# Optimization experiments

Measured on AMD Instinct MI355X. Metric: run time of the kernel, lower is better.

## Reference

```python
import jax, jax.numpy as jnp
import numpy as np

N = 131072
DIM = 16      # irrep dim of Rs_in == Rs_out (mul 4 of l=0,1)
YDIM = 9      # sum(2l+1) for l_filters {0,1,2}
NPATH = 96    # mul_dim of Rs_f (radial channels)
NPATH0 = 32   # linear (l=0) paths
HID = 64      # radial MLP hidden width


def _sh(u):
    """Real spherical harmonics for l=0,1,2 on unit vectors u[N,3] -> Y[9, N]."""
    x, y, z = u[:, 0], u[:, 1], u[:, 2]
    c0 = 0.28209479177387814
    c1 = 0.4886025119029199
    c2 = 1.0925484305920792
    return jnp.stack([
        jnp.full_like(x, c0),
        c1 * y, c1 * z, c1 * x,
        c2 * x * y,
        c2 * y * z,
        0.31539156525252005 * (3.0 * z * z - 1.0),
        c2 * x * z,
        0.5462742152960396 * (x * x - y * y),
    ])  # [YDIM, N]


def setup_inputs() -> dict:
    key = jax.random.key(0)
    ks = jax.random.split(key, 8)
    return {
        "r": jax.random.normal(ks[0], (N, 3), jnp.float32),
        "mixing_matrix1": jax.random.normal(ks[1], (DIM, DIM, YDIM, NPATH), jnp.float32) * 0.1,
        "mixing_matrix2": jax.random.normal(ks[2], (DIM, DIM, NPATH0), jnp.float32) * 0.1,
        "weight": jax.random.normal(ks[3], (NPATH0,), jnp.float32),
        "W1": jax.random.normal(ks[4], (1, HID), jnp.float32),
        "b1": jnp.zeros((HID,), jnp.float32),
        "W2": jax.random.normal(ks[5], (HID, NPATH), jnp.float32) / 8.0,
        "b2": jnp.zeros((NPATH,), jnp.float32),
    }


def reference(r, mixing_matrix1, mixing_matrix2, weight, W1, b1, W2, b2):
    r_eps = 0.0
    radii = jnp.linalg.norm(r, axis=1)                 # [N]
    mask = radii > r_eps                               # [N]
    u = r / jnp.maximum(radii, 1e-12)[:, None]         # unit vectors
    Y = _sh(u)                                         # [YDIM, N]
    # radial MLP: R -> R^NPATH
    h = jax.nn.relu(radii[:, None] @ W1 + b1)          # [N, HID]
    R = h @ W2 + b2                                    # [N, NPATH]
    # kernel1 = einsum('ijyw,yz,zw->zij'): outer(Y,R) per point, then one GEMM
    F = jnp.einsum('yz,zw->zyw', Y, R).reshape(-1, YDIM * NPATH)   # [N, y*w]
    k1 = (F @ mixing_matrix1.reshape(DIM * DIM, YDIM * NPATH).T).reshape(-1, DIM, DIM)
    # kernel2 = einsum('ijk,k->ij')
    k2 = jnp.einsum('ijk,k->ij', mixing_matrix2, weight)           # [DIM, DIM]
    # scatter: radii>eps gets kernel1, radii<=eps gets kernel2 (jit-safe select)
    return jnp.where(mask[:, None, None], k1, k2[None, :, :])      # [N, DIM, DIM]
```

## Files before the change

kernel.cpp:

```cpp
#include <hip/hip_runtime.h>
#include <math.h>

#define NPTS   131072
#define DIMC   256
#define YD     9
#define NPATHS 96
#define NPATH0 32
#define HID    64
#define NREG   65
#define QSTR   18

typedef float f32x4 __attribute__((ext_vector_type(4)));


__global__ __launch_bounds__(256) void precompute_kernel(
    const float* __restrict__ W1, const float* __restrict__ b1,
    const float* __restrict__ W2, const float* __restrict__ b2,
    const float* __restrict__ M1, const float* __restrict__ M2,
    const float* __restrict__ wgt,
    float* __restrict__ Q, float* __restrict__ xout, float* __restrict__ k2out)
{
    const int j   = blockIdx.x / 3;
    const int ys  = blockIdx.x % 3;
    const int tid = threadIdx.x;
    __shared__ __align__(16) float sx[HID];
    __shared__ __align__(16) float sa[HID], sb[HID];
    __shared__ __align__(16) float ssa[HID], ssb[HID];
    __shared__ __align__(16) float sv[NPATHS], sc[NPATHS];

    if (tid < HID) {
        float a = W1[tid], b = b1[tid];
        sa[tid] = a; sb[tid] = b;
        bool flips = (a > 0.f && b < 0.f) || (a < 0.f && b > 0.f);
        sx[tid] = flips ? (-b / a) : __builtin_inff();
    }
    __syncthreads();
    if (tid < HID) {
        float a = sa[tid], b = sb[tid], xh = sx[tid];
        int rank = 0;
        for (int k = 0; k < HID; ++k) {
            float xk = sx[k];
            rank += (xk < xh || (xk == xh && k < tid)) ? 1 : 0;
        }
        bool base = (b > 0.f) || (b == 0.f && a > 0.f);
        bool sig  = base ^ (rank < j);
        ssa[tid] = sig ? a : 0.f;
        ssb[tid] = sig ? b : 0.f;
    }
    __syncthreads();
    if (tid < NPATHS) {
        float vv = 0.f, cc = 0.f;
        for (int h = 0; h < HID; ++h) {
            float w2 = W2[h * NPATHS + tid];
            vv += ssa[h] * w2;
            cc += ssb[h] * w2;
        }
        sv[tid] = vv;
        sc[tid] = cc + b2[tid];
    }
    __syncthreads();
    {
        const int c  = tid;
        const int y0 = ys * 3;
        float accP[3] = {0.f, 0.f, 0.f};
        float accD[3] = {0.f, 0.f, 0.f};
        for (int w4 = 0; w4 < NPATHS / 4; ++w4) {
            float4 v4 = ((const float4*)sv)[w4];
            float4 c4 = ((const float4*)sc)[w4];
            #pragma unroll
            for (int e = 0; e < 3; ++e) {
                const float4 m4 = *(const float4*)(M1 + (size_t)(c * YD + y0 + e) * NPATHS + w4 * 4);
                accP[e] += m4.x * v4.x + m4.y * v4.y + m4.z * v4.z + m4.w * v4.w;
                accD[e] += m4.x * c4.x + m4.y * c4.y + m4.z * c4.z + m4.w * c4.w;
            }
        }
        float* qrow = Q + ((size_t)j * DIMC + c) * QSTR;
        #pragma unroll
        for (int e = 0; e < 3; ++e) {
            qrow[y0 + e]     = accP[e];
            qrow[9 + y0 + e] = accD[e];
        }
    }
    if (j == 0 && ys == 0) {
        if (tid < HID) xout[tid] = sx[tid];
        float s = 0.f;
        #pragma unroll
        for (int k = 0; k < NPATH0; ++k) s += M2[tid * NPATH0 + k] * wgt[k];
        k2out[tid] = s;
    }
}

__global__ __launch_bounds__(256, 2) void main_kernel(
    const float* __restrict__ r, const float* __restrict__ Q,
    const float* __restrict__ xflip, const float* __restrict__ k2,
    float* __restrict__ out)
{
    __shared__ __align__(16) float qArr[64 * 20];
    __shared__ int sUni, sJJ0;
    const int tid = threadIdx.x;
    const int n0  = blockIdx.x * 64;

    if (tid < 64) {
        const int n = n0 + tid;
        float rx = r[(size_t)n * 3 + 0];
        float ry = r[(size_t)n * 3 + 1];
        float rz = r[(size_t)n * 3 + 2];
        float t  = sqrtf(rx * rx + ry * ry + rz * rz);
        float rcp = 1.f / fmaxf(t, 1e-12f);
        float ux = rx * rcp, uy = ry * rcp, uz = rz * rcp;
        const float c0 = 0.28209479177387814f;
        const float c1 = 0.4886025119029199f;
        const float c2 = 1.0925484305920792f;
        float Y[9];
        Y[0] = c0;
        Y[1] = c1 * uy;
        Y[2] = c1 * uz;
        Y[3] = c1 * ux;
        Y[4] = c2 * ux * uy;
        Y[5] = c2 * uy * uz;
        Y[6] = 0.31539156525252005f * (3.f * uz * uz - 1.f);
        Y[7] = c2 * ux * uz;
        Y[8] = 0.5462742152960396f * (ux * ux - uy * uy);
        int jj = 0;
        for (int h = 0; h < HID; ++h) jj += (xflip[h] < t) ? 1 : 0;
        float* q = qArr + tid * 20;
        #pragma unroll
        for (int y = 0; y < 9; ++y) { q[y] = t * Y[y]; q[9 + y] = Y[y]; }
        q[18] = (float)jj;
        q[19] = (t > 0.f) ? 1.f : 0.f;
        int jj0 = __shfl(jj, 0, 64);
        unsigned long long bal = __ballot(jj == jj0);
        if (tid == 0) { sUni = (bal == 0xFFFFFFFFFFFFFFFFULL) ? 1 : 0; sJJ0 = jj0; }
    }
    __syncthreads();

    const int cg  = tid & 63;
    const int pg  = tid >> 6;
    const int c0i = cg * 4;
    const float4 k2v = *(const float4*)(k2 + c0i);
    const int pbeg = pg * 16;

    if (sUni) {
        const float4* cb = (const float4*)(Q + ((size_t)sJJ0 * DIMC + c0i) * QSTR);
        float cfs[72];
        #pragma unroll
        for (int v = 0; v < 18; ++v) {
            float4 t4 = cb[v];
            cfs[v * 4 + 0] = t4.x; cfs[v * 4 + 1] = t4.y;
            cfs[v * 4 + 2] = t4.z; cfs[v * 4 + 3] = t4.w;
        }
        for (int p = pbeg; p < pbeg + 16; ++p) {
            const float4* qv = (const float4*)(qArr + p * 20);
            float4 a0 = qv[0], a1 = qv[1], a2 = qv[2], a3 = qv[3], a4 = qv[4];
            float acc0, acc1, acc2, acc3;
            acc0  = a0.x * cfs[ 0] + a0.y * cfs[ 1] + a0.z * cfs[ 2] + a0.w * cfs[ 3];
            acc0 += a1.x * cfs[ 4] + a1.y * cfs[ 5] + a1.z * cfs[ 6] + a1.w * cfs[ 7];
            acc0 += a2.x * cfs[ 8] + a2.y * cfs[ 9] + a2.z * cfs[10] + a2.w * cfs[11];
            acc0 += a3.x * cfs[12] + a3.y * cfs[13] + a3.z * cfs[14] + a3.w * cfs[15];
            acc0 += a4.x * cfs[16] + a4.y * cfs[17];
            acc1  = a0.x * cfs[18] + a0.y * cfs[19] + a0.z * cfs[20] + a0.w * cfs[21];
            acc1 += a1.x * cfs[22] + a1.y * cfs[23] + a1.z * cfs[24] + a1.w * cfs[25];
            acc1 += a2.x * cfs[26] + a2.y * cfs[27] + a2.z * cfs[28] + a2.w * cfs[29];
            acc1 += a3.x * cfs[30] + a3.y * cfs[31] + a3.z * cfs[32] + a3.w * cfs[33];
            acc1 += a4.x * cfs[34] + a4.y * cfs[35];
            acc2  = a0.x * cfs[36] + a0.y * cfs[37] + a0.z * cfs[38] + a0.w * cfs[39];
            acc2 += a1.x * cfs[40] + a1.y * cfs[41] + a1.z * cfs[42] + a1.w * cfs[43];
            acc2 += a2.x * cfs[44] + a2.y * cfs[45] + a2.z * cfs[46] + a2.w * cfs[47];
            acc2 += a3.x * cfs[48] + a3.y * cfs[49] + a3.z * cfs[50] + a3.w * cfs[51];
            acc2 += a4.x * cfs[52] + a4.y * cfs[53];
            acc3  = a0.x * cfs[54] + a0.y * cfs[55] + a0.z * cfs[56] + a0.w * cfs[57];
            acc3 += a1.x * cfs[58] + a1.y * cfs[59] + a1.z * cfs[60] + a1.w * cfs[61];
            acc3 += a2.x * cfs[62] + a2.y * cfs[63] + a2.z * cfs[64] + a2.w * cfs[65];
            acc3 += a3.x * cfs[66] + a3.y * cfs[67] + a3.z * cfs[68] + a3.w * cfs[69];
            acc3 += a4.x * cfs[70] + a4.y * cfs[71];
            const bool msk = (a4.w != 0.f);
            f32x4 o;
            o.x = msk ? acc0 : k2v.x;
            o.y = msk ? acc1 : k2v.y;
            o.z = msk ? acc2 : k2v.z;
            o.w = msk ? acc3 : k2v.w;
            __builtin_nontemporal_store(o, (f32x4*)(out + (size_t)(n0 + p) * DIMC + c0i));
        }
    } else {
        float cfs[72];
        int curj = -1;
        for (int p = pbeg; p < pbeg + 16; ++p) {
            const float4* qv = (const float4*)(qArr + p * 20);
            float4 a0 = qv[0], a1 = qv[1], a2 = qv[2], a3 = qv[3], a4 = qv[4];
            int jj = (int)a4.z;
            if (jj != curj) {
                curj = jj;
                const float4* cb = (const float4*)(Q + ((size_t)jj * DIMC + c0i) * QSTR);
                #pragma unroll
                for (int v = 0; v < 18; ++v) {
                    float4 t4 = cb[v];
                    cfs[v * 4 + 0] = t4.x; cfs[v * 4 + 1] = t4.y;
                    cfs[v * 4 + 2] = t4.z; cfs[v * 4 + 3] = t4.w;
                }
            }
            float qs[18] = { a0.x, a0.y, a0.z, a0.w,  a1.x, a1.y, a1.z, a1.w,
                             a2.x, a2.y, a2.z, a2.w,  a3.x, a3.y, a3.z, a3.w,
                             a4.x, a4.y };
            float acc0 = 0.f, acc1 = 0.f, acc2 = 0.f, acc3 = 0.f;
            #pragma unroll
            for (int i = 0; i < 18; ++i) {
                acc0 += qs[i] * cfs[0 * 18 + i];
                acc1 += qs[i] * cfs[1 * 18 + i];
                acc2 += qs[i] * cfs[2 * 18 + i];
                acc3 += qs[i] * cfs[3 * 18 + i];
            }
            const bool msk = (a4.w != 0.f);
            float4 o;
            o.x = msk ? acc0 : k2v.x;
            o.y = msk ? acc1 : k2v.y;
            o.z = msk ? acc2 : k2v.z;
            o.w = msk ? acc3 : k2v.w;
            *(float4*)(out + (size_t)(n0 + p) * DIMC + c0i) = o;
        }
    }
}

extern "C" void kernel_launch(void* const* d_in, const int* in_sizes, int n_in,
                              void* d_out, int out_size, void* d_ws, size_t ws_size,
                              hipStream_t stream)
{
    const float* r   = (const float*)d_in[0];
    const float* M1  = (const float*)d_in[1];
    const float* M2  = (const float*)d_in[2];
    const float* wgt = (const float*)d_in[3];
    const float* W1  = (const float*)d_in[4];
    const float* b1  = (const float*)d_in[5];
    const float* W2  = (const float*)d_in[6];
    const float* b2  = (const float*)d_in[7];
    float* out = (float*)d_out;

    float* ws = (float*)d_ws;
    float* Q  = ws;
    float* xf = ws + (size_t)NREG * DIMC * QSTR;
    float* k2 = xf + HID;

    precompute_kernel<<<NREG * 3, 256, 0, stream>>>(W1, b1, W2, b2, M1, M2, wgt, Q, xf, k2);
    main_kernel<<<NPTS / 64, 256, 0, stream>>>(r, Q, xf, k2, out);
}
```

Before: 186.7 us.

## Transpose Q layout, coalesce precompute with shuffle reductions, prefetch coefficients before barrier

Precompute now has 8 lanes cooperatively dot each M1 row with the slope and intercept vectors, reduce with xor shuffles, and write Q in a transposed [region][y][channel] layout. The main kernel reads coefficients as coalesced float4 strided loads, speculatively loads region-0 coefficients before the barrier to overlap with the per-point setup, and caches flip points in LDS. It also raises the occupancy hint to 3 blocks per SM and uses nontemporal stores on the non-uniform path. The risk is extra register pressure from the higher launch bound and a wasted load when region 0 is not the one used.

Result: no change. 188.6 us (+1.0%).

```diff
diff --git a/kernel.cpp b/kernel.cpp
--- a/kernel.cpp
+++ b/kernel.cpp
@@ -20,9 +20,9 @@
     const float* __restrict__ wgt,
     float* __restrict__ Q, float* __restrict__ xout, float* __restrict__ k2out)
 {
-    const int j   = blockIdx.x / 3;
-    const int ys  = blockIdx.x % 3;
-    const int tid = threadIdx.x;
+    const int j    = blockIdx.x >> 2;
+    const int rblk = blockIdx.x & 3;
+    const int tid  = threadIdx.x;
     __shared__ __align__(16) float sx[HID];
     __shared__ __align__(16) float sa[HID], sb[HID];
     __shared__ __align__(16) float ssa[HID], ssb[HID];
@@ -59,29 +59,44 @@
         sc[tid] = cc + b2[tid];
     }
     __syncthreads();
+
     {
-        const int c  = tid;
-        const int y0 = ys * 3;
-        float accP[3] = {0.f, 0.f, 0.f};
-        float accD[3] = {0.f, 0.f, 0.f};
-        for (int w4 = 0; w4 < NPATHS / 4; ++w4) {
-            float4 v4 = ((const float4*)sv)[w4];
-            float4 c4 = ((const float4*)sc)[w4];
-            #pragma unroll
-            for (int e = 0; e < 3; ++e) {
-                const float4 m4 = *(const float4*)(M1 + (size_t)(c * YD + y0 + e) * NPATHS + w4 * 4);
-                accP[e] += m4.x * v4.x + m4.y * v4.y + m4.z * v4.z + m4.w * v4.w;
-                accD[e] += m4.x * c4.x + m4.y * c4.y + m4.z * c4.z + m4.w * c4.w;
-            }
-        }
-        float* qrow = Q + ((size_t)j * DIMC + c) * QSTR;
-        #pragma unroll
-        for (int e = 0; e < 3; ++e) {
-            qrow[y0 + e]     = accP[e];
-            qrow[9 + y0 + e] = accD[e];
-        }
-    }
-    if (j == 0 && ys == 0) {
+        const int g    = tid >> 3;
+        const int lane = tid & 7;
+        const float4 v0 = *(const float4*)(sv + lane * 4);
+        const float4 v1 = *(const float4*)(sv + lane * 4 + 32);
+        const float4 v2 = *(const float4*)(sv + lane * 4 + 64);
+        const float4 d0 = *(const float4*)(sc + lane * 4);
+        const float4 d1 = *(const float4*)(sc + lane * 4 + 32);
+        const float4 d2 = *(const float4*)(sc + lane * 4 + 64);
+        const int row0 = rblk * (2304 / 4);
+        for (int it = 0; it < (2304 / 4) / 32; ++it) {
+            const int row = row0 + it * 32 + g;
+            const float* mrow = M1 + (size_t)row * NPATHS + lane * 4;
+            float4 m0 = *(const float4*)(mrow);
+            float4 m1 = *(const float4*)(mrow + 32);
+            float4 m2 = *(const float4*)(mrow + 64);
+            float p = m0.x*v0.x + m0.y*v0.y + m0.z*v0.z + m0.w*v0.w
+                    + m1.x*v1.x + m1.y*v1.y + m1.z*v1.z + m1.w*v1.w
+                    + m2.x*v2.x + m2.y*v2.y + m2.z*v2.z + m2.w*v2.w;
+            float d = m0.x*d0.x + m0.y*d0.y + m0.z*d0.z + m0.w*d0.w
+                    + m1.x*d1.x + m1.y*d1.y + m1.z*d1.z + m1.w*d1.w
+                    + m2.x*d2.x + m2.y*d2.y + m2.z*d2.z + m2.w*d2.w;
+            #pragma unroll
+            for (int off = 1; off < 8; off <<= 1) {
+                p += __shfl_xor(p, off, 64);
+                d += __shfl_xor(d, off, 64);
+            }
+            if (lane == 0) {
+                const int c = row / 9;
+                const int y = row - c * 9;
+                Q[((size_t)j * QSTR + y)     * DIMC + c] = p;
+                Q[((size_t)j * QSTR + 9 + y) * DIMC + c] = d;
+            }
+        }
+    }
+
+    if (blockIdx.x == 0) {
         if (tid < HID) xout[tid] = sx[tid];
         float s = 0.f;
         #pragma unroll
@@ -90,17 +105,22 @@
     }
 }
 
-__global__ __launch_bounds__(256, 2) void main_kernel(
+__global__ __launch_bounds__(256, 3) void main_kernel(
     const float* __restrict__ r, const float* __restrict__ Q,
     const float* __restrict__ xflip, const float* __restrict__ k2,
     float* __restrict__ out)
 {
     __shared__ __align__(16) float qArr[64 * 20];
+    __shared__ __align__(16) float sxf[64];
     __shared__ int sUni, sJJ0;
     const int tid = threadIdx.x;
     const int n0  = blockIdx.x * 64;
+    const int cg  = tid & 63;
+    const int pg  = tid >> 6;
+    const int c0i = cg * 4;
 
     if (tid < 64) {
+        sxf[tid] = xflip[tid];
         const int n = n0 + tid;
         float rx = r[(size_t)n * 3 + 0];
         float ry = r[(size_t)n * 3 + 1];
@@ -121,58 +141,62 @@
         Y[6] = 0.31539156525252005f * (3.f * uz * uz - 1.f);
         Y[7] = c2 * ux * uz;
         Y[8] = 0.5462742152960396f * (ux * ux - uy * uy);
+        float* q = qArr + tid * 20;
+        #pragma unroll
+        for (int y = 0; y < 9; ++y) { q[y] = t * Y[y]; q[9 + y] = Y[y]; }
+        q[19] = (t > 0.f) ? 1.f : 0.f;
         int jj = 0;
-        for (int h = 0; h < HID; ++h) jj += (xflip[h] < t) ? 1 : 0;
-        float* q = qArr + tid * 20;
-        #pragma unroll
-        for (int y = 0; y < 9; ++y) { q[y] = t * Y[y]; q[9 + y] = Y[y]; }
+        #pragma unroll
+        for (int h4 = 0; h4 < 16; ++h4) {
+            float4 x4 = ((const float4*)sxf)[h4];
+            jj += (x4.x < t ? 1 : 0) + (x4.y < t ? 1 : 0)
+                + (x4.z < t ? 1 : 0) + (x4.w < t ? 1 : 0);
+        }
         q[18] = (float)jj;
-        q[19] = (t > 0.f) ? 1.f : 0.f;
         int jj0 = __shfl(jj, 0, 64);
         unsigned long long bal = __ballot(jj == jj0);
         if (tid == 0) { sUni = (bal == 0xFFFFFFFFFFFFFFFFULL) ? 1 : 0; sJJ0 = jj0; }
     }
-    __syncthreads();
-
-    const int cg  = tid & 63;
-    const int pg  = tid >> 6;
-    const int c0i = cg * 4;
+
+    float cfs[72];
+    {
+        const float4* cb = (const float4*)Q + cg;
+        #pragma unroll
+        for (int v = 0; v < 18; ++v) {
+            float4 t4 = cb[v * 64];
+            cfs[v * 4 + 0] = t4.x; cfs[v * 4 + 1] = t4.y;
+            cfs[v * 4 + 2] = t4.z; cfs[v * 4 + 3] = t4.w;
+        }
+    }
+    __syncthreads();
+
     const float4 k2v = *(const float4*)(k2 + c0i);
     const int pbeg = pg * 16;
 
     if (sUni) {
-        const float4* cb = (const float4*)(Q + ((size_t)sJJ0 * DIMC + c0i) * QSTR);
-        float cfs[72];
-        #pragma unroll
-        for (int v = 0; v < 18; ++v) {
-            float4 t4 = cb[v];
-            cfs[v * 4 + 0] = t4.x; cfs[v * 4 + 1] = t4.y;
-            cfs[v * 4 + 2] = t4.z; cfs[v * 4 + 3] = t4.w;
+        if (sJJ0 != 0) {
+            const float4* cb = (const float4*)(Q + (size_t)sJJ0 * QSTR * DIMC) + cg;
+            #pragma unroll
+            for (int v = 0; v < 18; ++v) {
+                float4 t4 = cb[v * 64];
+                cfs[v * 4 + 0] = t4.x; cfs[v * 4 + 1] = t4.y;
+                cfs[v * 4 + 2] = t4.z; cfs[v * 4 + 3] = t4.w;
+            }
         }
         for (int p = pbeg; p < pbeg + 16; ++p) {
             const float4* qv = (const float4*)(qArr + p * 20);
             float4 a0 = qv[0], a1 = qv[1], a2 = qv[2], a3 = qv[3], a4 = qv[4];
-            float acc0, acc1, acc2, acc3;
-            acc0  = a0.x * cfs[ 0] + a0.y * cfs[ 1] + a0.z * cfs[ 2] + a0.w * cfs[ 3];
-            acc0 += a1.x * cfs[ 4] + a1.y * cfs[ 5] + a1.z * cfs[ 6] + a1.w * cfs[ 7];
-            acc0 += a2.x * cfs[ 8] + a2.y * cfs[ 9] + a2.z * cfs[10] + a2.w * cfs[11];
-            acc0 += a3.x * cfs[12] + a3.y * cfs[13] + a3.z * cfs[14] + a3.w * cfs[15];
-            acc0 += a4.x * cfs[16] + a4.y * cfs[17];
-            acc1  = a0.x * cfs[18] + a0.y * cfs[19] + a0.z * cfs[20] + a0.w * cfs[21];
-            acc1 += a1.x * cfs[22] + a1.y * cfs[23] + a1.z * cfs[24] + a1.w * cfs[25];
-            acc1 += a2.x * cfs[26] + a2.y * cfs[27] + a2.z * cfs[28] + a2.w * cfs[29];
-            acc1 += a3.x * cfs[30] + a3.y * cfs[31] + a3.z * cfs[32] + a3.w * cfs[33];
-            acc1 += a4.x * cfs[34] + a4.y * cfs[35];
-            acc2  = a0.x * cfs[36] + a0.y * cfs[37] + a0.z * cfs[38] + a0.w * cfs[39];
-            acc2 += a1.x * cfs[40] + a1.y * cfs[41] + a1.z * cfs[42] + a1.w * cfs[43];
-            acc2 += a2.x * cfs[44] + a2.y * cfs[45] + a2.z * cfs[46] + a2.w * cfs[47];
-            acc2 += a3.x * cfs[48] + a3.y * cfs[49] + a3.z * cfs[50] + a3.w * cfs[51];
-            acc2 += a4.x * cfs[52] + a4.y * cfs[53];
-            acc3  = a0.x * cfs[54] + a0.y * cfs[55] + a0.z * cfs[56] + a0.w * cfs[57];
-            acc3 += a1.x * cfs[58] + a1.y * cfs[59] + a1.z * cfs[60] + a1.w * cfs[61];
-            acc3 += a2.x * cfs[62] + a2.y * cfs[63] + a2.z * cfs[64] + a2.w * cfs[65];
-            acc3 += a3.x * cfs[66] + a3.y * cfs[67] + a3.z * cfs[68] + a3.w * cfs[69];
-            acc3 += a4.x * cfs[70] + a4.y * cfs[71];
+            const float qs[18] = { a0.x, a0.y, a0.z, a0.w,  a1.x, a1.y, a1.z, a1.w,
+                                   a2.x, a2.y, a2.z, a2.w,  a3.x, a3.y, a3.z, a3.w,
+                                   a4.x, a4.y };
+            float acc0 = 0.f, acc1 = 0.f, acc2 = 0.f, acc3 = 0.f;
+            #pragma unroll
+            for (int v = 0; v < 18; ++v) {
+                acc0 += qs[v] * cfs[v * 4 + 0];
+                acc1 += qs[v] * cfs[v * 4 + 1];
+                acc2 += qs[v] * cfs[v * 4 + 2];
+                acc3 += qs[v] * cfs[v * 4 + 3];
+            }
             const bool msk = (a4.w != 0.f);
             f32x4 o;
             o.x = msk ? acc0 : k2v.x;
@@ -182,40 +206,39 @@
             __builtin_nontemporal_store(o, (f32x4*)(out + (size_t)(n0 + p) * DIMC + c0i));
         }
     } else {
-        float cfs[72];
-        int curj = -1;
+        int curj = 0;
         for (int p = pbeg; p < pbeg + 16; ++p) {
             const float4* qv = (const float4*)(qArr + p * 20);
             float4 a0 = qv[0], a1 = qv[1], a2 = qv[2], a3 = qv[3], a4 = qv[4];
             int jj = (int)a4.z;
             if (jj != curj) {
                 curj = jj;
-                const float4* cb = (const float4*)(Q + ((size_t)jj * DIMC + c0i) * QSTR);
+                const float4* cb = (const float4*)(Q + (size_t)jj * QSTR * DIMC) + cg;
                 #pragma unroll
                 for (int v = 0; v < 18; ++v) {
-                    float4 t4 = cb[v];
+                    float4 t4 = cb[v * 64];
                     cfs[v * 4 + 0] = t4.x; cfs[v * 4 + 1] = t4.y;
                     cfs[v * 4 + 2] = t4.z; cfs[v * 4 + 3] = t4.w;
                 }
             }
-            float qs[18] = { a0.x, a0.y, a0.z, a0.w,  a1.x, a1.y, a1.z, a1.w,
-                             a2.x, a2.y, a2.z, a2.w,  a3.x, a3.y, a3.z, a3.w,
-                             a4.x, a4.y };
+            const float qs[18] = { a0.x, a0.y, a0.z, a0.w,  a1.x, a1.y, a1.z, a1.w,
+                                   a2.x, a2.y, a2.z, a2.w,  a3.x, a3.y, a3.z, a3.w,
+                                   a4.x, a4.y };
             float acc0 = 0.f, acc1 = 0.f, acc2 = 0.f, acc3 = 0.f;
             #pragma unroll
-            for (int i = 0; i < 18; ++i) {
-                acc0 += qs[i] * cfs[0 * 18 + i];
-                acc1 += qs[i] * cfs[1 * 18 + i];
-                acc2 += qs[i] * cfs[2 * 18 + i];
-                acc3 += qs[i] * cfs[3 * 18 + i];
+            for (int v = 0; v < 18; ++v) {
+                acc0 += qs[v] * cfs[v * 4 + 0];
+                acc1 += qs[v] * cfs[v * 4 + 1];
+                acc2 += qs[v] * cfs[v * 4 + 2];
+                acc3 += qs[v] * cfs[v * 4 + 3];
             }
             const bool msk = (a4.w != 0.f);
-            float4 o;
+            f32x4 o;
             o.x = msk ? acc0 : k2v.x;
             o.y = msk ? acc1 : k2v.y;
             o.z = msk ? acc2 : k2v.z;
             o.w = msk ? acc3 : k2v.w;
-            *(float4*)(out + (size_t)(n0 + p) * DIMC + c0i) = o;
+            __builtin_nontemporal_store(o, (f32x4*)(out + (size_t)(n0 + p) * DIMC + c0i));
         }
     }
 }
@@ -239,6 +262,6 @@
     float* xf = ws + (size_t)NREG * DIMC * QSTR;
     float* k2 = xf + HID;
 
-    precompute_kernel<<<NREG * 3, 256, 0, stream>>>(W1, b1, W2, b2, M1, M2, wgt, Q, xf, k2);
+    precompute_kernel<<<NREG * 4, 256, 0, stream>>>(W1, b1, W2, b2, M1, M2, wgt, Q, xf, k2);
     main_kernel<<<NPTS / 64, 256, 0, stream>>>(r, Q, xf, k2, out);
 }
```
